# Kernel tuning notes

Measured on AMD Instinct MI355X. Metric: run time of the kernel, lower is better.

## Reference

```python
import jax, jax.numpy as jnp
import numpy as np

B, S, H = 2, 112, 768
M = 256     # cfg.mlp_hidden_size
L = 54      # vocab size of 'ent_rel_id' (joint labels)
O = 10      # ent_rel_file['q_num_logits']


def setup_inputs() -> dict:
    key = jax.random.key(0)
    ks = jax.random.split(key, 12)
    inp = {
        "seq_encoder_reprs": jax.random.normal(ks[0], (B, S, H), jnp.float32),
        "joint_label_matrix": jax.random.randint(ks[1], (B, S, S), 0, L),
        "joint_label_matrix_mask": jax.random.randint(ks[2], (B, S, S), 0, 2) > 0,
        "quintuplet_matrix": jax.random.randint(ks[3], (B, S, S, S), 0, O),
        "quintuplet_matrix_mask": jax.random.randint(ks[4], (B, S, S, S), 0, 2) > 0,
        # learned parameters (BertLinear = Linear + activation; dropout inactive at eval)
        "pair_w": jax.random.normal(ks[5], (2 * H, M), jnp.float32) * 0.02,
        "pair_b": jnp.zeros((M,), jnp.float32),
        "final_w": jax.random.normal(ks[6], (M, L), jnp.float32) * 0.02,
        "final_b": jnp.zeros((L,), jnp.float32),
        "value_w": jax.random.normal(ks[7], (H, M), jnp.float32) * 0.02,
        "value_b": jnp.zeros((M,), jnp.float32),
        # U is zero-initialized in the module; use small random values so the
        # triaffine path produces non-trivial numerics.
        "U": jax.random.normal(ks[8], (O, M, M), jnp.float32) * 0.02,
    }
    return inp


def _masked_ce(logits, labels, mask):
    # mean cross-entropy over masked positions (== CE over boolean-indexed rows)
    logp = jax.nn.log_softmax(logits, axis=-1)
    nll = -jnp.take_along_axis(logp, labels[..., None], axis=-1)[..., 0]
    m = mask.astype(logits.dtype)
    return jnp.sum(nll * m) / jnp.maximum(jnp.sum(m), 1.0)


def reference(seq_encoder_reprs, joint_label_matrix, joint_label_matrix_mask,
              quintuplet_matrix, quintuplet_matrix_mask,
              pair_w, pair_b, final_w, final_b, value_w, value_b, U):
    x = seq_encoder_reprs  # [B,S,H]
    # pair = cat(head_expand, tail_expand) -> pair_mlp (Linear + GELU)
    # split the Linear over the concat to avoid materializing [B,S,S,2H]:
    # cat([head,tail]) @ W == head @ W[:H] + tail @ W[H:]
    h_part = jnp.einsum('bxh,hm->bxm', x, pair_w[:H])   # head contribution
    t_part = jnp.einsum('byh,hm->bym', x, pair_w[H:])   # tail contribution
    pair = jax.nn.gelu(h_part[:, :, None, :] + t_part[:, None, :, :] + pair_b,
                       approximate=False)               # [B,S,S,M]
    joint_score = jnp.einsum('bxym,ml->bxyl', pair, final_w) + final_b  # [B,S,S,L]

    value = jax.nn.gelu(jnp.einsum('bzh,hm->bzm', x, value_w) + value_b,
                        approximate=False)              # [B,S,M]
    # triaffine: bxyi,oij,bzj->bxyzo ; contract value with U first (small interm.)
    vU = jnp.einsum('bzj,oij->bzoi', value, U)          # [B,S,O,M]
    q_score = jnp.einsum('bxyi,bzoi->bxyzo', pair, vU)  # [B,S,S,S,O]

    # q_loss: CrossEntropy applied to softmax(q_score) (as in the source)
    q_probs = jax.nn.softmax(q_score, axis=-1)
    q_loss = _masked_ce(q_probs, quintuplet_matrix, quintuplet_matrix_mask)
    element_loss = _masked_ce(joint_score, joint_label_matrix, joint_label_matrix_mask)
    loss = element_loss + q_loss
    return loss, joint_score, q_score
```

## Files before the change

### kernel.cpp

```cpp
#include <hip/hip_runtime.h>
#include <hip/hip_bf16.h>

#define BB 2
#define SS 112
#define HH 768
#define MM 256
#define LL 54
#define OO 10
#define NPAIR (BB*SS*SS)
#define NQPOS (BB*SS*SS*SS)
#define SO (SS*OO)
#define SOP 1152
#define S2 (SS*SS)
#define NQBLK (NQPOS/512)
#define NJBLK (NPAIR/128)

typedef short bf16x8 __attribute__((ext_vector_type(8)));
typedef float f32x4 __attribute__((ext_vector_type(4)));

#define WS_HP    64
#define WS_TP    57408
#define WS_VAL   114752
#define WS_UT    172096
#define WS_VUB   827456
#define WS_PAIRB 1122368
#define WS_FWB   4333632
#define WS_QPART 4341824
#define WS_EPART 4352800

__device__ __forceinline__ float gelu_exact(float v) {
    return 0.5f * v * (1.0f + erff(v * 0.70710678118654752f));
}

__global__ __launch_bounds__(256) void k_pre(const float* __restrict__ x,
                                             const float* __restrict__ pw,
                                             const float* __restrict__ vw,
                                             const float* __restrict__ vb,
                                             const float* __restrict__ U,
                                             const float* __restrict__ fw,
                                             float* __restrict__ hp,
                                             float* __restrict__ tp,
                                             float* __restrict__ val,
                                             float* __restrict__ UT,
                                             __hip_bfloat16* __restrict__ fwb) {
    __shared__ float sm[1056];
    const int id = blockIdx.x;
    const int tid = threadIdx.x;
    if (id < 672) {
        const int row = id % 224, sel = id / 224;
        const float* xr = x + (long)row * HH;
        for (int i = tid; i < HH; i += 256) sm[i] = xr[i];
        __syncthreads();
        const int m = tid;
        const float* w = (sel == 0) ? pw : (sel == 1) ? (pw + (long)HH * MM) : vw;
        float a = 0.f;
        for (int h = 0; h < HH; ++h)
            a = fmaf(sm[h], w[(long)h * MM + m], a);
        if (sel == 0)      hp[(long)row * MM + m] = a;
        else if (sel == 1) tp[(long)row * MM + m] = a;
        else               val[(long)row * MM + m] = gelu_exact(a + vb[m]);
    } else if (id < 1312) {
        const int t = id - 672;
        const int o = t / 64, rest = t % 64;
        const int i0 = (rest >> 3) * 32, j0 = (rest & 7) * 32;
        const int tx = tid & 31, ty = tid >> 5;
        float (*tt)[33] = (float(*)[33])sm;
        for (int r = 0; r < 32; r += 8)
            tt[ty + r][tx] = U[((long)(o * MM + i0 + ty + r)) * MM + j0 + tx];
        __syncthreads();
        for (int r = 0; r < 32; r += 8)
            UT[((long)(o * MM + j0 + ty + r)) * MM + i0 + tx] = tt[tx][ty + r];
    } else {
        const int idx2 = (id - 1312) * 256 + tid;
        const int c = idx2 >> 8, k = idx2 & 255;
        const float v = (c < LL) ? fw[(long)k * LL + c] : 0.f;
        fwb[idx2] = __float2bfloat16(v);
    }
}

__global__ __launch_bounds__(256) void k_mid(const float* __restrict__ val,
                                             const float* __restrict__ UT,
                                             __hip_bfloat16* __restrict__ vub,
                                             const float* __restrict__ hp,
                                             const float* __restrict__ tp,
                                             const float* __restrict__ pb,
                                             __hip_bfloat16* __restrict__ pairb) {
    __shared__ float sm[8 * MM];
    const int id = blockIdx.x;
    const int tid = threadIdx.x;
    if (id < 280) {
        const int b = id / 140, r = id % 140;
        const int o = r / 14, zt = r % 14;
        const int z0 = zt * 8;
        float (*vs)[MM] = (float(*)[MM])sm;
        for (int idx = tid; idx < 8 * MM; idx += 256) {
            const int zz = idx >> 8, m = idx & 255;
            vs[zz][m] = val[((long)(b * SS + z0 + zz)) * MM + m];
        }
        __syncthreads();
        const int i = tid;
        float acc[8];
#pragma unroll
        for (int zz = 0; zz < 8; ++zz) acc[zz] = 0.f;
        const float* utp = UT + (long)o * MM * MM + i;
        for (int j = 0; j < MM; ++j) {
            const float u = utp[(long)j * MM];
#pragma unroll
            for (int zz = 0; zz < 8; ++zz) acc[zz] = fmaf(vs[zz][j], u, acc[zz]);
        }
#pragma unroll
        for (int zz = 0; zz < 8; ++zz)
            vub[((long)b * SOP + (z0 + zz) * OO + o) * MM + i] = __float2bfloat16(acc[zz]);
    } else {
        const int p = id - 280;
        const int bx = p % 224;
        const int y0base = (p / 224) * 56;
        sm[tid] = hp[(long)bx * MM + tid] + pb[tid];
        __syncthreads();
        const int b = bx / SS;
        const int half = tid >> 7;
        const int m0 = (tid & 127) * 2;
        const float h0 = sm[m0], h1 = sm[m0 + 1];
        for (int y0 = y0base; y0 < y0base + 56; y0 += 2) {
            const int y = y0 + half;
            const float2 t2 = *(const float2*)(tp + ((long)(b * SS + y)) * MM + m0);
            __hip_bfloat162 o2;
            o2.x = __float2bfloat16(gelu_exact(h0 + t2.x));
            o2.y = __float2bfloat16(gelu_exact(h1 + t2.y));
            *(__hip_bfloat162*)(pairb + ((long)bx * SS + y) * MM + m0) = o2;
        }
    }
}

__device__ __forceinline__ void reduce2_part(float v1, float v2, float* slot) {
    const int lane = threadIdx.x & 63, wid = threadIdx.x >> 6;
#pragma unroll
    for (int off = 32; off > 0; off >>= 1) {
        v1 += __shfl_down(v1, off, 64);
        v2 += __shfl_down(v2, off, 64);
    }
    __shared__ float w1[4], w2[4];
    if (lane == 0) { w1[wid] = v1; w2[wid] = v2; }
    __syncthreads();
    if (threadIdx.x == 0) {
        slot[0] = w1[0] + w1[1] + w1[2] + w1[3];
        slot[1] = w2[0] + w2[1] + w2[2] + w2[3];
    }
}

__global__ __launch_bounds__(256) void k_jointg(const __hip_bfloat16* __restrict__ pairb,
                                                const __hip_bfloat16* __restrict__ fwb,
                                                const float* __restrict__ fb,
                                                const int* __restrict__ jlab,
                                                const int* __restrict__ jmask,
                                                float* __restrict__ joint,
                                                float* __restrict__ epart) {
    __shared__ __align__(16) char smem[33280];
    char* Al = smem;
    char* Bl = smem + 16384;
    const int r0 = blockIdx.x * 128;
    const int tid = threadIdx.x;
    const int lane = tid & 63, wid = tid >> 6;
    const int rl = lane & 15, kb = lane >> 4;

    int arow[4], aci[4], wadA[4];
#pragma unroll
    for (int j = 0; j < 4; ++j) {
        const int chunk = tid + 256 * j;
        arow[j] = chunk >> 3; aci[j] = chunk & 7;
        wadA[j] = (arow[j] * 128 + aci[j] * 16) ^ ((arow[j] & 7) << 4);
    }
    int brow[2], bci[2], wadB[2];
#pragma unroll
    for (int j = 0; j < 2; ++j) {
        const int chunk = tid + 256 * j;
        brow[j] = chunk >> 3; bci[j] = chunk & 7;
        wadB[j] = (brow[j] * 128 + bci[j] * 16) ^ ((brow[j] & 7) << 4);
    }

    f32x4 acc[2][4] = {};
    float4 ra[4], rb[2];

    auto issue = [&](int kt) {
#pragma unroll
        for (int j = 0; j < 4; ++j)
            ra[j] = *(const float4*)((const char*)pairb +
                     ((long)(r0 + arow[j]) * MM + kt * 64 + aci[j] * 8) * 2);
#pragma unroll
        for (int j = 0; j < 2; ++j)
            rb[j] = *(const float4*)((const char*)fwb +
                     ((long)brow[j] * MM + kt * 64 + bci[j] * 8) * 2);
    };
    auto dowrite = [&]() {
#pragma unroll
        for (int j = 0; j < 4; ++j) *(float4*)(Al + wadA[j]) = ra[j];
#pragma unroll
        for (int j = 0; j < 2; ++j) *(float4*)(Bl + wadB[j]) = rb[j];
    };
    auto compute = [&]() {
#pragma unroll
        for (int ks = 0; ks < 2; ++ks) {
            bf16x8 af[2], bv[4];
#pragma unroll
            for (int m = 0; m < 2; ++m) {
                const int rr = wid * 32 + m * 16 + rl;
                af[m] = *(const bf16x8*)(Al + ((rr * 128 + ks * 64 + kb * 16) ^ ((rr & 7) << 4)));
            }
#pragma unroll
            for (int n = 0; n < 4; ++n) {
                const int cc = n * 16 + rl;
                bv[n] = *(const bf16x8*)(Bl + ((cc * 128 + ks * 64 + kb * 16) ^ ((cc & 7) << 4)));
            }
#pragma unroll
            for (int m = 0; m < 2; ++m)
#pragma unroll
                for (int n = 0; n < 4; ++n)
                    acc[m][n] = __builtin_amdgcn_mfma_f32_16x16x32_bf16(af[m], bv[n], acc[m][n], 0, 0, 0);
        }
    };

    issue(0); dowrite(); __syncthreads();
    for (int kt = 0; kt < 4; ++kt) {
        if (kt < 3) issue(kt + 1);
        compute();
        __syncthreads();
        if (kt < 3) { dowrite(); __syncthreads(); }
    }

    float* stage = (float*)smem;
    __syncthreads();
#pragma unroll
    for (int m = 0; m < 2; ++m)
#pragma unroll
        for (int n = 0; n < 4; ++n) {
            const int col = n * 16 + rl;
            const float bias = (col < LL) ? fb[col] : 0.f;
            const int lrow0 = wid * 32 + m * 16 + kb * 4;
#pragma unroll
            for (int j = 0; j < 4; ++j) {
                const float v = acc[m][n][j] + bias;
                if (col < LL)
                    joint[(long)(r0 + lrow0 + j) * LL + col] = v;
                stage[(lrow0 + j) * 65 + col] = v;
            }
        }
    __syncthreads();

    float nll = 0.f, cnt = 0.f;
    if (tid < 128) {
        const int gi = r0 + tid;
        if (jmask[gi] != 0) {
            const float* s = stage + tid * 65;
            float mx = -3.4e38f;
            for (int l = 0; l < LL; ++l) mx = fmaxf(mx, s[l]);
            float se = 0.f;
            for (int l = 0; l < LL; ++l) se += expf(s[l] - mx);
            nll = mx + logf(se) - s[jlab[gi]];
            cnt = 1.f;
        }
    }
    reduce2_part(nll, cnt, epart + 2 * blockIdx.x);
}

__global__ __launch_bounds__(256) void k_qgemm(const __hip_bfloat16* __restrict__ pairb,
                                               const __hip_bfloat16* __restrict__ vub,
                                               float* __restrict__ qout) {
    __shared__ __align__(16) char Al[16384];
    __shared__ __align__(16) char Bl[16384];
    const int b = blockIdx.z;
    const int r0 = blockIdx.y * 128;
    const int c0 = blockIdx.x * 128;
    const __hip_bfloat16* A  = pairb + (long)b * S2 * MM;
    const __hip_bfloat16* Bm = vub + (long)b * SOP * MM;
    const int tid = threadIdx.x;
    const int lane = tid & 63, wid = tid >> 6;
    const int wr = wid >> 1, wc = wid & 1;
    const int rl = lane & 15, kb = lane >> 4;

    int arow[4], aci[4], wad[4];
#pragma unroll
    for (int j = 0; j < 4; ++j) {
        const int chunk = tid + 256 * j;
        arow[j] = chunk >> 3; aci[j] = chunk & 7;
        wad[j] = (arow[j] * 128 + aci[j] * 16) ^ ((arow[j] & 7) << 4);
    }

    f32x4 acc[4][4] = {};
    float4 ra[4], rb[4];

    auto issue = [&](int kt) {
#pragma unroll
        for (int j = 0; j < 4; ++j) {
            ra[j] = *(const float4*)((const char*)A +
                     ((long)(r0 + arow[j]) * MM + kt * 64 + aci[j] * 8) * 2);
            rb[j] = *(const float4*)((const char*)Bm +
                     ((long)(c0 + arow[j]) * MM + kt * 64 + aci[j] * 8) * 2);
        }
    };
    auto dowrite = [&]() {
#pragma unroll
        for (int j = 0; j < 4; ++j) {
            *(float4*)(Al + wad[j]) = ra[j];
            *(float4*)(Bl + wad[j]) = rb[j];
        }
    };
    auto compute = [&]() {
#pragma unroll
        for (int ks = 0; ks < 2; ++ks) {
            bf16x8 af[4], bv[4];
#pragma unroll
            for (int m = 0; m < 4; ++m) {
                const int rr = wr * 64 + m * 16 + rl;
                af[m] = *(const bf16x8*)(Al + ((rr * 128 + ks * 64 + kb * 16) ^ ((rr & 7) << 4)));
            }
#pragma unroll
            for (int n = 0; n < 4; ++n) {
                const int cc = wc * 64 + n * 16 + rl;
                bv[n] = *(const bf16x8*)(Bl + ((cc * 128 + ks * 64 + kb * 16) ^ ((cc & 7) << 4)));
            }
#pragma unroll
            for (int m = 0; m < 4; ++m)
#pragma unroll
                for (int n = 0; n < 4; ++n)
                    acc[m][n] = __builtin_amdgcn_mfma_f32_16x16x32_bf16(af[m], bv[n], acc[m][n], 0, 0, 0);
        }
    };

    issue(0); dowrite(); __syncthreads();
    for (int kt = 0; kt < 4; ++kt) {
        if (kt < 3) issue(kt + 1);
        compute();
        __syncthreads();
        if (kt < 3) { dowrite(); __syncthreads(); }
    }

    float* C = qout + (long)b * S2 * SO;
#pragma unroll
    for (int m = 0; m < 4; ++m)
#pragma unroll
        for (int n = 0; n < 4; ++n) {
            const int col = c0 + wc * 64 + n * 16 + rl;
            if (col < SO) {
                const int rbase = r0 + wr * 64 + m * 16 + kb * 4;
#pragma unroll
                for (int j = 0; j < 4; ++j)
                    C[(long)(rbase + j) * SO + col] = acc[m][n][j];
            }
        }
}

__global__ __launch_bounds__(256) void k_qloss(const float* __restrict__ q,
                                               const int* __restrict__ labels,
                                               const int* __restrict__ mask,
                                               float* __restrict__ qpart) {
    __shared__ float qs[512 * 11];
    const int base = blockIdx.x * 512;
    const float* src = q + (long)base * OO;
    for (int i = threadIdx.x; i < 512 * OO; i += 256) {
        const int p = i / 10, o = i - p * 10;
        qs[p * 11 + o] = src[i];
    }
    __syncthreads();
    float nll = 0.f, cnt = 0.f;
#pragma unroll
    for (int j = 0; j < 2; ++j) {
        const int p = threadIdx.x + 256 * j;
        const int gi = base + p;
        if (mask[gi] != 0) {
            const float* s = qs + p * 11;
            float r[OO];
#pragma unroll
            for (int o = 0; o < OO; ++o) r[o] = s[o];
            float mx = r[0];
#pragma unroll
            for (int o = 1; o < OO; ++o) mx = fmaxf(mx, r[o]);
            float se = 0.f;
#pragma unroll
            for (int o = 0; o < OO; ++o) { r[o] = expf(r[o] - mx); se += r[o]; }
            const float inv = 1.0f / se;
            float se2 = 0.f;
#pragma unroll
            for (int o = 0; o < OO; ++o) se2 += expf(r[o] * inv);
            const float plab = expf(s[labels[gi]] - mx) * inv;
            nll += logf(se2) - plab;
            cnt += 1.f;
        }
    }
    reduce2_part(nll, cnt, qpart + 2 * blockIdx.x);
}

__global__ __launch_bounds__(256) void k_final(const float* __restrict__ qpart,
                                               const float* __restrict__ epart,
                                               float* __restrict__ out) {
    __shared__ float s1[256], s2[256], s3[256], s4[256];
    float q1 = 0.f, q2 = 0.f, e1 = 0.f, e2 = 0.f;
    for (int i = threadIdx.x; i < NQBLK; i += 256) {
        q1 += qpart[2 * i]; q2 += qpart[2 * i + 1];
    }
    for (int i = threadIdx.x; i < NJBLK; i += 256) {
        e1 += epart[2 * i]; e2 += epart[2 * i + 1];
    }
    const int t = threadIdx.x;
    s1[t] = q1; s2[t] = q2; s3[t] = e1; s4[t] = e2;
    __syncthreads();
    for (int off = 128; off > 0; off >>= 1) {
        if (t < off) {
            s1[t] += s1[t + off]; s2[t] += s2[t + off];
            s3[t] += s3[t + off]; s4[t] += s4[t + off];
        }
        __syncthreads();
    }
    if (t == 0)
        out[0] = s3[0] / fmaxf(s4[0], 1.0f) + s1[0] / fmaxf(s2[0], 1.0f);
}

extern "C" void kernel_launch(void* const* d_in, const int* in_sizes, int n_in,
                              void* d_out, int out_size, void* d_ws, size_t ws_size,
                              hipStream_t stream) {
    const float* x     = (const float*)d_in[0];
    const int*   jlab  = (const int*)d_in[1];
    const int*   jmask = (const int*)d_in[2];
    const int*   qlab  = (const int*)d_in[3];
    const int*   qmask = (const int*)d_in[4];
    const float* pw    = (const float*)d_in[5];
    const float* pb    = (const float*)d_in[6];
    const float* fw    = (const float*)d_in[7];
    const float* fb    = (const float*)d_in[8];
    const float* vw    = (const float*)d_in[9];
    const float* vb    = (const float*)d_in[10];
    const float* U     = (const float*)d_in[11];

    float* out  = (float*)d_out;
    float* ws   = (float*)d_ws;
    float* hp   = ws + WS_HP;
    float* tp   = ws + WS_TP;
    float* val  = ws + WS_VAL;
    float* UT   = ws + WS_UT;
    __hip_bfloat16* vub   = (__hip_bfloat16*)(ws + WS_VUB);
    __hip_bfloat16* pairb = (__hip_bfloat16*)(ws + WS_PAIRB);
    __hip_bfloat16* fwb   = (__hip_bfloat16*)(ws + WS_FWB);
    float* qpart = ws + WS_QPART;
    float* epart = ws + WS_EPART;

    float* joint = out + 1;
    float* qsc   = out + 1 + (long)NPAIR * LL;

    k_pre<<<1376, 256, 0, stream>>>(x, pw, vw, vb, U, fw, hp, tp, val, UT, fwb);
    k_mid<<<728, 256, 0, stream>>>(val, UT, vub, hp, tp, pb, pairb);
    k_jointg<<<NJBLK, 256, 0, stream>>>(pairb, fwb, fb, jlab, jmask, joint, epart);
    k_qgemm<<<dim3(9, 98, BB), 256, 0, stream>>>(pairb, vub, qsc);
    k_qloss<<<NQBLK, 256, 0, stream>>>(qsc, qlab, qmask, qpart);
    k_final<<<1, 256, 0, stream>>>(qpart, epart, out);
}
```

Before: 184.3 us.

## Merge joint and triaffine GEMMs into one launch; fold final reduction into qloss

Combines the joint-score GEMM and the q-score GEMM into a single kernel whose blocks branch on block index, so the small joint GEMM shares the GPU with the large q GEMM and one launch boundary goes away. The separate final-reduction kernel is removed: the last k_qloss block, found through an atomic ticket counter reset by a memset, sums the partial losses. The joint staging stride also shrinks and padded columns are skipped. This adds a memset launch and a threadfence/atomic step, and the ticket pattern depends on correct memory ordering.

```diff
diff --git a/kernel.cpp b/kernel.cpp
--- a/kernel.cpp
+++ b/kernel.cpp
@@ -14,10 +14,12 @@
 #define S2 (SS*SS)
 #define NQBLK (NQPOS/512)
 #define NJBLK (NPAIR/128)
+#define NHEAVY (NJBLK + 9*98*BB)
 
 typedef short bf16x8 __attribute__((ext_vector_type(8)));
 typedef float f32x4 __attribute__((ext_vector_type(4)));
 
+#define WS_CNT   0
 #define WS_HP    64
 #define WS_TP    57408
 #define WS_VAL   114752
@@ -148,211 +150,214 @@
     }
 }
 
-__global__ __launch_bounds__(256) void k_jointg(const __hip_bfloat16* __restrict__ pairb,
-                                                const __hip_bfloat16* __restrict__ fwb,
-                                                const float* __restrict__ fb,
-                                                const int* __restrict__ jlab,
-                                                const int* __restrict__ jmask,
-                                                float* __restrict__ joint,
-                                                float* __restrict__ epart) {
-    __shared__ __align__(16) char smem[33280];
+__global__ __launch_bounds__(256) void k_heavy(const __hip_bfloat16* __restrict__ pairb,
+                                               const __hip_bfloat16* __restrict__ fwb,
+                                               const float* __restrict__ fb,
+                                               const int* __restrict__ jlab,
+                                               const int* __restrict__ jmask,
+                                               float* __restrict__ joint,
+                                               float* __restrict__ epart,
+                                               const __hip_bfloat16* __restrict__ vub,
+                                               float* __restrict__ qout) {
+    __shared__ __align__(16) char smem[32768];
     char* Al = smem;
-    char* Bl = smem + 16384;
-    const int r0 = blockIdx.x * 128;
+    const int id = blockIdx.x;
     const int tid = threadIdx.x;
     const int lane = tid & 63, wid = tid >> 6;
     const int rl = lane & 15, kb = lane >> 4;
 
-    int arow[4], aci[4], wadA[4];
-#pragma unroll
-    for (int j = 0; j < 4; ++j) {
-        const int chunk = tid + 256 * j;
-        arow[j] = chunk >> 3; aci[j] = chunk & 7;
-        wadA[j] = (arow[j] * 128 + aci[j] * 16) ^ ((arow[j] & 7) << 4);
-    }
-    int brow[2], bci[2], wadB[2];
-#pragma unroll
-    for (int j = 0; j < 2; ++j) {
-        const int chunk = tid + 256 * j;
-        brow[j] = chunk >> 3; bci[j] = chunk & 7;
-        wadB[j] = (brow[j] * 128 + bci[j] * 16) ^ ((brow[j] & 7) << 4);
-    }
-
-    f32x4 acc[2][4] = {};
-    float4 ra[4], rb[2];
-
-    auto issue = [&](int kt) {
-#pragma unroll
-        for (int j = 0; j < 4; ++j)
-            ra[j] = *(const float4*)((const char*)pairb +
-                     ((long)(r0 + arow[j]) * MM + kt * 64 + aci[j] * 8) * 2);
-#pragma unroll
-        for (int j = 0; j < 2; ++j)
-            rb[j] = *(const float4*)((const char*)fwb +
-                     ((long)brow[j] * MM + kt * 64 + bci[j] * 8) * 2);
-    };
-    auto dowrite = [&]() {
-#pragma unroll
-        for (int j = 0; j < 4; ++j) *(float4*)(Al + wadA[j]) = ra[j];
-#pragma unroll
-        for (int j = 0; j < 2; ++j) *(float4*)(Bl + wadB[j]) = rb[j];
-    };
-    auto compute = [&]() {
-#pragma unroll
-        for (int ks = 0; ks < 2; ++ks) {
-            bf16x8 af[2], bv[4];
-#pragma unroll
-            for (int m = 0; m < 2; ++m) {
-                const int rr = wid * 32 + m * 16 + rl;
-                af[m] = *(const bf16x8*)(Al + ((rr * 128 + ks * 64 + kb * 16) ^ ((rr & 7) << 4)));
-            }
+    if (id < NJBLK) {
+        char* Bl = smem + 16384;
+        const int r0 = id * 128;
+
+        int arow[4], aci[4], wadA[4];
+#pragma unroll
+        for (int j = 0; j < 4; ++j) {
+            const int chunk = tid + 256 * j;
+            arow[j] = chunk >> 3; aci[j] = chunk & 7;
+            wadA[j] = (arow[j] * 128 + aci[j] * 16) ^ ((arow[j] & 7) << 4);
+        }
+        int brow[2], bci[2], wadB[2];
+#pragma unroll
+        for (int j = 0; j < 2; ++j) {
+            const int chunk = tid + 256 * j;
+            brow[j] = chunk >> 3; bci[j] = chunk & 7;
+            wadB[j] = (brow[j] * 128 + bci[j] * 16) ^ ((brow[j] & 7) << 4);
+        }
+
+        f32x4 acc[2][4] = {};
+        float4 ra[4], rb[2];
+
+        auto issue = [&](int kt) {
+#pragma unroll
+            for (int j = 0; j < 4; ++j)
+                ra[j] = *(const float4*)((const char*)pairb +
+                         ((long)(r0 + arow[j]) * MM + kt * 64 + aci[j] * 8) * 2);
+#pragma unroll
+            for (int j = 0; j < 2; ++j)
+                rb[j] = *(const float4*)((const char*)fwb +
+                         ((long)brow[j] * MM + kt * 64 + bci[j] * 8) * 2);
+        };
+        auto dowrite = [&]() {
+#pragma unroll
+            for (int j = 0; j < 4; ++j) *(float4*)(Al + wadA[j]) = ra[j];
+#pragma unroll
+            for (int j = 0; j < 2; ++j) *(float4*)(Bl + wadB[j]) = rb[j];
+        };
+        auto compute = [&]() {
+#pragma unroll
+            for (int ks = 0; ks < 2; ++ks) {
+                bf16x8 af[2], bv[4];
+#pragma unroll
+                for (int m = 0; m < 2; ++m) {
+                    const int rr = wid * 32 + m * 16 + rl;
+                    af[m] = *(const bf16x8*)(Al + ((rr * 128 + ks * 64 + kb * 16) ^ ((rr & 7) << 4)));
+                }
+#pragma unroll
+                for (int n = 0; n < 4; ++n) {
+                    const int cc = n * 16 + rl;
+                    bv[n] = *(const bf16x8*)(Bl + ((cc * 128 + ks * 64 + kb * 16) ^ ((cc & 7) << 4)));
+                }
+#pragma unroll
+                for (int m = 0; m < 2; ++m)
+#pragma unroll
+                    for (int n = 0; n < 4; ++n)
+                        acc[m][n] = __builtin_amdgcn_mfma_f32_16x16x32_bf16(af[m], bv[n], acc[m][n], 0, 0, 0);
+            }
+        };
+
+        issue(0); dowrite(); __syncthreads();
+        for (int kt = 0; kt < 4; ++kt) {
+            if (kt < 3) issue(kt + 1);
+            compute();
+            __syncthreads();
+            if (kt < 3) { dowrite(); __syncthreads(); }
+        }
+
+        float* stage = (float*)smem;
+        __syncthreads();
+#pragma unroll
+        for (int m = 0; m < 2; ++m)
 #pragma unroll
             for (int n = 0; n < 4; ++n) {
-                const int cc = n * 16 + rl;
-                bv[n] = *(const bf16x8*)(Bl + ((cc * 128 + ks * 64 + kb * 16) ^ ((cc & 7) << 4)));
-            }
-#pragma unroll
-            for (int m = 0; m < 2; ++m)
-#pragma unroll
-                for (int n = 0; n < 4; ++n)
-                    acc[m][n] = __builtin_amdgcn_mfma_f32_16x16x32_bf16(af[m], bv[n], acc[m][n], 0, 0, 0);
-        }
-    };
-
-    issue(0); dowrite(); __syncthreads();
-    for (int kt = 0; kt < 4; ++kt) {
-        if (kt < 3) issue(kt + 1);
-        compute();
-        __syncthreads();
-        if (kt < 3) { dowrite(); __syncthreads(); }
-    }
-
-    float* stage = (float*)smem;
-    __syncthreads();
-#pragma unroll
-    for (int m = 0; m < 2; ++m)
-#pragma unroll
-        for (int n = 0; n < 4; ++n) {
-            const int col = n * 16 + rl;
-            const float bias = (col < LL) ? fb[col] : 0.f;
-            const int lrow0 = wid * 32 + m * 16 + kb * 4;
+                const int col = n * 16 + rl;
+                if (col < LL) {
+                    const float bias = fb[col];
+                    const int lrow0 = wid * 32 + m * 16 + kb * 4;
+#pragma unroll
+                    for (int j = 0; j < 4; ++j) {
+                        const float v = acc[m][n][j] + bias;
+                        joint[(long)(r0 + lrow0 + j) * LL + col] = v;
+                        stage[(lrow0 + j) * 55 + col] = v;
+                    }
+                }
+            }
+        __syncthreads();
+
+        float nll = 0.f, cnt = 0.f;
+        if (tid < 128) {
+            const int gi = r0 + tid;
+            if (jmask[gi] != 0) {
+                const float* s = stage + tid * 55;
+                float mx = -3.4e38f;
+                for (int l = 0; l < LL; ++l) mx = fmaxf(mx, s[l]);
+                float se = 0.f;
+                for (int l = 0; l < LL; ++l) se += expf(s[l] - mx);
+                nll = mx + logf(se) - s[jlab[gi]];
+                cnt = 1.f;
+            }
+        }
+        reduce2_part(nll, cnt, epart + 2 * id);
+    } else {
+        char* Bl = smem + 16384;
+        const int qid = id - NJBLK;
+        const int c0 = (qid % 9) * 128;
+        const int r0 = ((qid / 9) % 98) * 128;
+        const int b = qid / (9 * 98);
+        const __hip_bfloat16* A  = pairb + (long)b * S2 * MM;
+        const __hip_bfloat16* Bm = vub + (long)b * SOP * MM;
+        const int wr = wid >> 1, wc = wid & 1;
+
+        int arow[4], aci[4], wad[4];
+#pragma unroll
+        for (int j = 0; j < 4; ++j) {
+            const int chunk = tid + 256 * j;
+            arow[j] = chunk >> 3; aci[j] = chunk & 7;
+            wad[j] = (arow[j] * 128 + aci[j] * 16) ^ ((arow[j] & 7) << 4);
+        }
+
+        f32x4 acc[4][4] = {};
+        float4 ra[4], rb[4];
+
+        auto issue = [&](int kt) {
 #pragma unroll
             for (int j = 0; j < 4; ++j) {
-                const float v = acc[m][n][j] + bias;
-                if (col < LL)
-                    joint[(long)(r0 + lrow0 + j) * LL + col] = v;
-                stage[(lrow0 + j) * 65 + col] = v;
-            }
-        }
-    __syncthreads();
-
-    float nll = 0.f, cnt = 0.f;
-    if (tid < 128) {
-        const int gi = r0 + tid;
-        if (jmask[gi] != 0) {
-            const float* s = stage + tid * 65;
-            float mx = -3.4e38f;
-            for (int l = 0; l < LL; ++l) mx = fmaxf(mx, s[l]);
-            float se = 0.f;
-            for (int l = 0; l < LL; ++l) se += expf(s[l] - mx);
-            nll = mx + logf(se) - s[jlab[gi]];
-            cnt = 1.f;
-        }
-    }
-    reduce2_part(nll, cnt, epart + 2 * blockIdx.x);
-}
-
-__global__ __launch_bounds__(256) void k_qgemm(const __hip_bfloat16* __restrict__ pairb,
-                                               const __hip_bfloat16* __restrict__ vub,
-                                               float* __restrict__ qout) {
-    __shared__ __align__(16) char Al[16384];
-    __shared__ __align__(16) char Bl[16384];
-    const int b = blockIdx.z;
-    const int r0 = blockIdx.y * 128;
-    const int c0 = blockIdx.x * 128;
-    const __hip_bfloat16* A  = pairb + (long)b * S2 * MM;
-    const __hip_bfloat16* Bm = vub + (long)b * SOP * MM;
-    const int tid = threadIdx.x;
-    const int lane = tid & 63, wid = tid >> 6;
-    const int wr = wid >> 1, wc = wid & 1;
-    const int rl = lane & 15, kb = lane >> 4;
-
-    int arow[4], aci[4], wad[4];
-#pragma unroll
-    for (int j = 0; j < 4; ++j) {
-        const int chunk = tid + 256 * j;
-        arow[j] = chunk >> 3; aci[j] = chunk & 7;
-        wad[j] = (arow[j] * 128 + aci[j] * 16) ^ ((arow[j] & 7) << 4);
-    }
-
-    f32x4 acc[4][4] = {};
-    float4 ra[4], rb[4];
-
-    auto issue = [&](int kt) {
-#pragma unroll
-        for (int j = 0; j < 4; ++j) {
-            ra[j] = *(const float4*)((const char*)A +
-                     ((long)(r0 + arow[j]) * MM + kt * 64 + aci[j] * 8) * 2);
-            rb[j] = *(const float4*)((const char*)Bm +
-                     ((long)(c0 + arow[j]) * MM + kt * 64 + aci[j] * 8) * 2);
-        }
-    };
-    auto dowrite = [&]() {
-#pragma unroll
-        for (int j = 0; j < 4; ++j) {
-            *(float4*)(Al + wad[j]) = ra[j];
-            *(float4*)(Bl + wad[j]) = rb[j];
-        }
-    };
-    auto compute = [&]() {
-#pragma unroll
-        for (int ks = 0; ks < 2; ++ks) {
-            bf16x8 af[4], bv[4];
-#pragma unroll
-            for (int m = 0; m < 4; ++m) {
-                const int rr = wr * 64 + m * 16 + rl;
-                af[m] = *(const bf16x8*)(Al + ((rr * 128 + ks * 64 + kb * 16) ^ ((rr & 7) << 4)));
-            }
+                ra[j] = *(const float4*)((const char*)A +
+                         ((long)(r0 + arow[j]) * MM + kt * 64 + aci[j] * 8) * 2);
+                rb[j] = *(const float4*)((const char*)Bm +
+                         ((long)(c0 + arow[j]) * MM + kt * 64 + aci[j] * 8) * 2);
+            }
+        };
+        auto dowrite = [&]() {
+#pragma unroll
+            for (int j = 0; j < 4; ++j) {
+                *(float4*)(Al + wad[j]) = ra[j];
+                *(float4*)(Bl + wad[j]) = rb[j];
+            }
+        };
+        auto compute = [&]() {
+#pragma unroll
+            for (int ks = 0; ks < 2; ++ks) {
+                bf16x8 af[4], bv[4];
+#pragma unroll
+                for (int m = 0; m < 4; ++m) {
+                    const int rr = wr * 64 + m * 16 + rl;
+                    af[m] = *(const bf16x8*)(Al + ((rr * 128 + ks * 64 + kb * 16) ^ ((rr & 7) << 4)));
+                }
+#pragma unroll
+                for (int n = 0; n < 4; ++n) {
+                    const int cc = wc * 64 + n * 16 + rl;
+                    bv[n] = *(const bf16x8*)(Bl + ((cc * 128 + ks * 64 + kb * 16) ^ ((cc & 7) << 4)));
+                }
+#pragma unroll
+                for (int m = 0; m < 4; ++m)
+#pragma unroll
+                    for (int n = 0; n < 4; ++n)
+                        acc[m][n] = __builtin_amdgcn_mfma_f32_16x16x32_bf16(af[m], bv[n], acc[m][n], 0, 0, 0);
+            }
+        };
+
+        issue(0); dowrite(); __syncthreads();
+        for (int kt = 0; kt < 4; ++kt) {
+            if (kt < 3) issue(kt + 1);
+            compute();
+            __syncthreads();
+            if (kt < 3) { dowrite(); __syncthreads(); }
+        }
+
+        float* C = qout + (long)b * S2 * SO;
+#pragma unroll
+        for (int m = 0; m < 4; ++m)
 #pragma unroll
             for (int n = 0; n < 4; ++n) {
-                const int cc = wc * 64 + n * 16 + rl;
-                bv[n] = *(const bf16x8*)(Bl + ((cc * 128 + ks * 64 + kb * 16) ^ ((cc & 7) << 4)));
-            }
-#pragma unroll
-            for (int m = 0; m < 4; ++m)
-#pragma unroll
-                for (int n = 0; n < 4; ++n)
-                    acc[m][n] = __builtin_amdgcn_mfma_f32_16x16x32_bf16(af[m], bv[n], acc[m][n], 0, 0, 0);
-        }
-    };
-
-    issue(0); dowrite(); __syncthreads();
-    for (int kt = 0; kt < 4; ++kt) {
-        if (kt < 3) issue(kt + 1);
-        compute();
-        __syncthreads();
-        if (kt < 3) { dowrite(); __syncthreads(); }
-    }
-
-    float* C = qout + (long)b * S2 * SO;
-#pragma unroll
-    for (int m = 0; m < 4; ++m)
-#pragma unroll
-        for (int n = 0; n < 4; ++n) {
-            const int col = c0 + wc * 64 + n * 16 + rl;
-            if (col < SO) {
-                const int rbase = r0 + wr * 64 + m * 16 + kb * 4;
-#pragma unroll
-                for (int j = 0; j < 4; ++j)
-                    C[(long)(rbase + j) * SO + col] = acc[m][n][j];
-            }
-        }
+                const int col = c0 + wc * 64 + n * 16 + rl;
+                if (col < SO) {
+                    const int rbase = r0 + wr * 64 + m * 16 + kb * 4;
+#pragma unroll
+                    for (int j = 0; j < 4; ++j)
+                        C[(long)(rbase + j) * SO + col] = acc[m][n][j];
+                }
+            }
+    }
 }
 
 __global__ __launch_bounds__(256) void k_qloss(const float* __restrict__ q,
                                                const int* __restrict__ labels,
                                                const int* __restrict__ mask,
-                                               float* __restrict__ qpart) {
+                                               float* __restrict__ qpart,
+                                               const float* __restrict__ epart,
+                                               float* __restrict__ out,
+                                               unsigned* __restrict__ cnt_dev) {
     __shared__ float qs[512 * 11];
     const int base = blockIdx.x * 512;
     const float* src = q + (long)base * OO;
@@ -387,31 +392,34 @@
         }
     }
     reduce2_part(nll, cnt, qpart + 2 * blockIdx.x);
-}
-
-__global__ __launch_bounds__(256) void k_final(const float* __restrict__ qpart,
-                                               const float* __restrict__ epart,
-                                               float* __restrict__ out) {
-    __shared__ float s1[256], s2[256], s3[256], s4[256];
-    float q1 = 0.f, q2 = 0.f, e1 = 0.f, e2 = 0.f;
-    for (int i = threadIdx.x; i < NQBLK; i += 256) {
-        q1 += qpart[2 * i]; q2 += qpart[2 * i + 1];
-    }
-    for (int i = threadIdx.x; i < NJBLK; i += 256) {
-        e1 += epart[2 * i]; e2 += epart[2 * i + 1];
-    }
-    const int t = threadIdx.x;
-    s1[t] = q1; s2[t] = q2; s3[t] = e1; s4[t] = e2;
+
+    __threadfence();
+    __shared__ unsigned ticket;
+    if (threadIdx.x == 0) ticket = atomicAdd(cnt_dev, 1u);
     __syncthreads();
-    for (int off = 128; off > 0; off >>= 1) {
-        if (t < off) {
-            s1[t] += s1[t + off]; s2[t] += s2[t + off];
-            s3[t] += s3[t + off]; s4[t] += s4[t + off];
-        }
-        __syncthreads();
-    }
-    if (t == 0)
-        out[0] = s3[0] / fmaxf(s4[0], 1.0f) + s1[0] / fmaxf(s2[0], 1.0f);
+    if (ticket == NQBLK - 1) {
+        __threadfence();
+        __shared__ float s1[256], s2[256], s3[256], s4[256];
+        float q1 = 0.f, q2 = 0.f, e1 = 0.f, e2 = 0.f;
+        for (int i = threadIdx.x; i < NQBLK; i += 256) {
+            q1 += qpart[2 * i]; q2 += qpart[2 * i + 1];
+        }
+        for (int i = threadIdx.x; i < 196; i += 256) {
+            e1 += epart[2 * i]; e2 += epart[2 * i + 1];
+        }
+        const int t = threadIdx.x;
+        s1[t] = q1; s2[t] = q2; s3[t] = e1; s4[t] = e2;
+        __syncthreads();
+        for (int off = 128; off > 0; off >>= 1) {
+            if (t < off) {
+                s1[t] += s1[t + off]; s2[t] += s2[t + off];
+                s3[t] += s3[t + off]; s4[t] += s4[t + off];
+            }
+            __syncthreads();
+        }
+        if (t == 0)
+            out[0] = s3[0] / fmaxf(s4[0], 1.0f) + s1[0] / fmaxf(s2[0], 1.0f);
+    }
 }
 
 extern "C" void kernel_launch(void* const* d_in, const int* in_sizes, int n_in,
@@ -432,6 +440,7 @@
 
     float* out  = (float*)d_out;
     float* ws   = (float*)d_ws;
+    unsigned* cnt_dev = (unsigned*)(ws + WS_CNT);
     float* hp   = ws + WS_HP;
     float* tp   = ws + WS_TP;
     float* val  = ws + WS_VAL;
@@ -445,10 +454,9 @@
     float* joint = out + 1;
     float* qsc   = out + 1 + (long)NPAIR * LL;
 
+    hipMemsetAsync(cnt_dev, 0, sizeof(unsigned), stream);
     k_pre<<<1376, 256, 0, stream>>>(x, pw, vw, vb, U, fw, hp, tp, val, UT, fwb);
     k_mid<<<728, 256, 0, stream>>>(val, UT, vub, hp, tp, pb, pairb);
-    k_jointg<<<NJBLK, 256, 0, stream>>>(pairb, fwb, fb, jlab, jmask, joint, epart);
-    k_qgemm<<<dim3(9, 98, BB), 256, 0, stream>>>(pairb, vub, qsc);
-    k_qloss<<<NQBLK, 256, 0, stream>>>(qsc, qlab, qmask, qpart);
-    k_final<<<1, 256, 0, stream>>>(qpart, epart, out);
-}
+    k_heavy<<<NHEAVY, 256, 0, stream>>>(pairb, fwb, fb, jlab, jmask, joint, epart, vub, qsc);
+    k_qloss<<<NQBLK, 256, 0, stream>>>(qsc, qlab, qmask, qpart, epart, out, cnt_dev);
+}
```

Result: slower. 678.6 us (+268.2%).
